# Optimization experiments

Measured on AMD Instinct MI355X. Metric: run time of the kernel, lower is better.

The kernel has to match this reference:

```python
import jax, jax.numpy as jnp
import numpy as np

B, V, D, NH, DH = 1, 6, 256, 8, 32
L, ZP = 4, 4
BEV = 80
Q = BEV * BEV
SHAPES = [(56, 100), (28, 50), (14, 25), (7, 13)]
N = sum(h * w for h, w in SHAPES)
PAD_H, PAD_W = 448, 800
PC = (-48.0, -48.0, -5.0, 48.0, 48.0, 3.0)
EPS = 1e-5


def _ref3d():
    # get_reference_points + pc_range scaling; the original overwrites the z channel
    # with scaled-x (code bug: ref_3d[...,2:3] = ref_3d[...,:1]*zrange+zmin) -> reproduced faithfully,
    # so all ZP pillar points are identical.
    u = jnp.arange(Q)
    xs = ((u % BEV).astype(jnp.float32) + 0.5) / BEV
    ys = ((u // BEV).astype(jnp.float32) + 0.5) / BEV
    x = xs * (PC[3] - PC[0]) + PC[0]
    y = ys * (PC[4] - PC[1]) + PC[1]
    z = x * (PC[5] - PC[2]) + PC[2]
    p = jnp.stack([x, y, z], -1)  # [Q,3]
    return jnp.broadcast_to(p[None], (ZP, Q, 3))


def _project(l2i):
    # l2i: [B,V,4,4] -> normalized coords [B,V,Q,ZP,2], validity mask [B,V,Q,ZP]
    pts = _ref3d().reshape(-1, 3)
    pts_h = jnp.concatenate([pts, jnp.ones_like(pts[:, :1])], -1)  # [ZP*Q,4]
    ip = jnp.einsum('bvij,nj->bvni', l2i, pts_h)                   # [B,V,ZP*Q,4]
    zc = ip[..., 2]
    xy = ip[..., :2] / jnp.clip(zc, EPS, None)[..., None]
    xn = xy[..., 0] / PAD_W
    yn = xy[..., 1] / PAD_H
    m = (zc > EPS) & (xn > 0) & (xn < 1) & (yn > 0) & (yn < 1)
    coords = jnp.stack([xn, yn], -1).reshape(B, V, ZP, Q, 2).transpose(0, 1, 3, 2, 4)
    mask = m.reshape(B, V, ZP, Q).transpose(0, 1, 3, 2)
    return coords, mask


def _forward(feat0, feat1, feat2, feat3, lidar2img_mat, bev_emb, level_embeds,
             view_embeds, value_W, value_b, off_W, off_b, aw_W, aw_b, out_W, out_b):
    feats = [feat0, feat1, feat2, feat3]
    parts = []
    for l, f in enumerate(feats):
        h, w = SHAPES[l]
        x = f.reshape(B, V, D, h * w).transpose(0, 1, 3, 2)  # [B,V,hw,D]
        x = x + view_embeds[None, :, None, :] + level_embeds[l]
        parts.append(x)
    feat_flat = jnp.concatenate(parts, axis=2)  # [B,V,N,D]

    coords, mask = _project(lidar2img_mat)
    mask_any = mask.any(-1)                                            # [B,V,Q]
    count = jnp.clip(mask_any.sum(1).astype(jnp.float32), 1.0, None)   # [B,Q]

    value = (feat_flat.reshape(B * V, N, D) @ value_W + value_b).reshape(B * V, N, NH, DH)
    off = (bev_emb @ off_W + off_b).reshape(Q, NH, L, ZP, 2)
    aw = jax.nn.softmax((bev_emb @ aw_W + aw_b).reshape(Q, NH, L * ZP), -1).reshape(Q, NH, L, ZP)
    ref = coords.reshape(B * V, Q, ZP, 2)

    out = jnp.zeros((B * V, Q, NH, DH), feat_flat.dtype)
    start = 0
    for l, (h, w) in enumerate(SHAPES):
        v_l = value[:, start:start + h * w].transpose(0, 2, 1, 3).reshape(B * V * NH, h * w, DH)
        start += h * w
        loc = ref[:, :, None, :, :] + off[None, :, :, l] / jnp.array([w, h], feat_flat.dtype)
        loc = loc.transpose(0, 2, 1, 3, 4).reshape(B * V * NH, Q * ZP, 2)
        # grid_sample(align_corners=False, padding='zeros') with grid 2*loc-1
        gx = loc[..., 0] * w - 0.5
        gy = loc[..., 1] * h - 0.5
        x0 = jnp.floor(gx).astype(jnp.int32)
        y0 = jnp.floor(gy).astype(jnp.int32)
        wx1 = gx - x0
        wy1 = gy - y0

        def corner(xi, yi, wt):
            valid = (xi >= 0) & (xi < w) & (yi >= 0) & (yi < h)
            lin = jnp.clip(yi, 0, h - 1) * w + jnp.clip(xi, 0, w - 1)
            g = jnp.take_along_axis(v_l, lin[..., None], axis=1)
            return g * (wt * valid)[..., None]

        s = (corner(x0, y0, (1 - wx1) * (1 - wy1)) + corner(x0 + 1, y0, wx1 * (1 - wy1))
             + corner(x0, y0 + 1, (1 - wx1) * wy1) + corner(x0 + 1, y0 + 1, wx1 * wy1))
        s = s.reshape(B * V, NH, Q, ZP, DH)
        out = out + jnp.einsum('vhqzd,qhz->vqhd', s, aw[:, :, l])

    attn = out.reshape(B, V, Q, D)
    slots = (attn * mask_any[..., None]).sum(1) / count[..., None]
    slots = slots @ out_W + out_b
    return bev_emb[None] + slots  # dropout is identity at inference


def setup_inputs() -> dict:
    key = jax.random.key(0)
    ks = jax.random.split(key, 16)
    s = 0.02
    return {
        'feat0': jax.random.normal(ks[0], (B, V, D) + SHAPES[0], jnp.float32),
        'feat1': jax.random.normal(ks[1], (B, V, D) + SHAPES[1], jnp.float32),
        'feat2': jax.random.normal(ks[2], (B, V, D) + SHAPES[2], jnp.float32),
        'feat3': jax.random.normal(ks[3], (B, V, D) + SHAPES[3], jnp.float32),
        'lidar2img_mat': jax.random.normal(ks[4], (B, V, 4, 4), jnp.float32) * 50.0,
        'bev_emb': jax.random.normal(ks[5], (Q, D), jnp.float32) * s,
        'level_embeds': jax.random.normal(ks[6], (L, D), jnp.float32) * s,
        'view_embeds': jax.random.normal(ks[7], (V, D), jnp.float32) * s,
        'value_W': jax.random.normal(ks[8], (D, D), jnp.float32) * s,
        'value_b': jnp.zeros((D,), jnp.float32),
        'off_W': jax.random.normal(ks[9], (D, NH * L * ZP * 2), jnp.float32) * s,
        'off_b': jnp.zeros((NH * L * ZP * 2,), jnp.float32),
        'aw_W': jax.random.normal(ks[10], (D, NH * L * ZP), jnp.float32) * s,
        'aw_b': jnp.zeros((NH * L * ZP,), jnp.float32),
        'out_W': jax.random.normal(ks[11], (D, D), jnp.float32) * s,
        'out_b': jnp.zeros((D,), jnp.float32),
    }


def reference(feat0, feat1, feat2, feat3, lidar2img_mat, bev_emb, level_embeds,
              view_embeds, value_W, value_b, off_W, off_b, aw_W, aw_b, out_W, out_b):
    return _forward(feat0, feat1, feat2, feat3, lidar2img_mat, bev_emb, level_embeds,
                    view_embeds, value_W, value_b, off_W, off_b, aw_W, aw_b, out_W, out_b)
```

## Files before the change

### kernel.cpp

```cpp
#include <hip/hip_runtime.h>
#include <cstdint>
#include <cstddef>

#define NV 6
#define ND 256
#define NHEAD 8
#define NBEV 80
#define NQ 6400
#define NTOK 7441
#define MROWS (NV * NTOK)
#define FEPS 1e-5f

typedef __attribute__((ext_vector_type(8))) short bfx8;
typedef __attribute__((ext_vector_type(4))) float fx4;

__device__ __forceinline__ unsigned short f2bf(float x) {
    uint32_t u = __builtin_bit_cast(uint32_t, x);
    u += 0x7FFFu + ((u >> 16) & 1u);
    return (unsigned short)(u >> 16);
}
__device__ __forceinline__ float lof(uint32_t u) {
    return __builtin_bit_cast(float, u << 16);
}
__device__ __forceinline__ float hif(uint32_t u) {
    return __builtin_bit_cast(float, u & 0xFFFF0000u);
}

__global__ __launch_bounds__(256) void k_prep(
        const float* __restrict__ l2i, const float* __restrict__ ve,
        const float* __restrict__ le, const float* __restrict__ vW,
        const float* __restrict__ vB, const float* __restrict__ oW,
        const float* __restrict__ aW, const float* __restrict__ outW,
        float2* __restrict__ coords, int* __restrict__ mask,
        unsigned short* __restrict__ vWt, unsigned short* __restrict__ oaWt,
        unsigned short* __restrict__ outWt, float* __restrict__ emb_proj) {
    int bid = blockIdx.x;
    int t = threadIdx.x;
    if (bid < 150) {
        int idx = bid * 256 + t;
        int v = idx / NQ, q = idx - v * NQ;
        float xs = ((float)(q % NBEV) + 0.5f) / (float)NBEV;
        float ys = ((float)(q / NBEV) + 0.5f) / (float)NBEV;
        float x = xs * 96.0f - 48.0f;
        float y = ys * 96.0f - 48.0f;
        float z = x * 8.0f - 5.0f;
        const float* M = l2i + v * 16;
        float ip0 = M[0] * x + M[1] * y + M[2] * z + M[3];
        float ip1 = M[4] * x + M[5] * y + M[6] * z + M[7];
        float ip2 = M[8] * x + M[9] * y + M[10] * z + M[11];
        float dz = fmaxf(ip2, FEPS);
        float xn = ip0 / dz / 800.0f;
        float yn = ip1 / dz / 448.0f;
        bool m = (ip2 > FEPS) && (xn > 0.0f) && (xn < 1.0f) && (yn > 0.0f) && (yn < 1.0f);
        coords[idx] = make_float2(xn, yn);
        mask[idx] = m ? 1 : 0;
    } else if (bid < 406) {
        int e = (bid - 150) * 256 + t;
        int n = e >> 8, k = e & 255;
        vWt[(size_t)n * 256 + k] = f2bf(vW[(size_t)k * 256 + n]);
    } else if (bid < 662) {
        int e = (bid - 406) * 256 + t;
        int n = e >> 8, k = e & 255;
        oaWt[(size_t)n * 256 + k] = f2bf(oW[(size_t)k * 256 + n]);
    } else if (bid < 790) {
        int e = (bid - 662) * 256 + t;
        int n = e >> 8, k = e & 255;
        oaWt[(size_t)(256 + n) * 256 + k] = f2bf(aW[(size_t)k * 128 + n]);
    } else if (bid < 1046) {
        int e = (bid - 790) * 256 + t;
        int n = e >> 8, k = e & 255;
        outWt[(size_t)n * 256 + k] = f2bf(outW[(size_t)k * 256 + n]);
    } else {
        int blk = bid - 1046;
        int v = blk >> 2, l = blk & 3;
        float acc = vB[t];
        for (int d = 0; d < ND; ++d)
            acc += (ve[v * ND + d] + le[l * ND + d]) * vW[d * ND + t];
        emb_proj[blk * ND + t] = acc;
    }
}

__global__ __launch_bounds__(256) void k_gemms(
        const float* __restrict__ f0, const float* __restrict__ f1,
        const float* __restrict__ f2, const float* __restrict__ f3,
        const unsigned short* __restrict__ vWt, const float* __restrict__ emb_proj,
        unsigned short* __restrict__ value,
        const float* __restrict__ bev, const unsigned short* __restrict__ oaWt,
        const float* __restrict__ oB, const float* __restrict__ aB,
        float* __restrict__ off, float* __restrict__ aw_pre) {
    __shared__ unsigned short As[128][40];
    __shared__ unsigned short Bs[128][40];
    __shared__ const float* rowptr[128];
    __shared__ int rowstride[128];
    __shared__ int rowemb[128];
    int bid = blockIdx.x;
    int t = threadIdx.x;
    int lane = t & 63, w = t >> 6;
    int wm = w >> 1, wn = w & 1;
    int lr = lane & 15, lk = lane >> 4;

    fx4 acc[4][4];
#pragma unroll
    for (int i = 0; i < 4; ++i)
#pragma unroll
        for (int j = 0; j < 4; ++j) acc[i][j] = (fx4)0.0f;

    if (bid < 698) {
        int m0 = (bid >> 1) * 128, c0 = (bid & 1) * 128;
        if (t < 128) {
            int m = m0 + t;
            if (m >= MROWS) m = MROWS - 1;
            int v = m / NTOK, n = m - v * NTOK;
            int l, p, hw;
            const float* base;
            if (n < 5600)      { l = 0; p = n;        hw = 5600; base = f0; }
            else if (n < 7000) { l = 1; p = n - 5600; hw = 1400; base = f1; }
            else if (n < 7350) { l = 2; p = n - 7000; hw = 350;  base = f2; }
            else               { l = 3; p = n - 7350; hw = 91;   base = f3; }
            rowptr[t] = base + (size_t)v * ND * hw + p;
            rowstride[t] = hw;
            rowemb[t] = v * 4 + l;
        }
        __syncthreads();
        int mA = t & 127, kg = t >> 7;
        const unsigned short* bp = vWt + (size_t)(c0 + (t >> 1)) * 256 + (t & 1) * 16;
        int br = t >> 1, bc = (t & 1) * 16;
        const float* rp = rowptr[mA];
        int rs = rowstride[mA];
        for (int k0 = 0; k0 < 256; k0 += 32) {
            float va[16];
#pragma unroll
            for (int i = 0; i < 16; ++i)
                va[i] = rp[(size_t)(k0 + kg * 16 + i) * rs];
            bfx8 lo8, hi8;
#pragma unroll
            for (int i = 0; i < 8; ++i) {
                lo8[i] = (short)f2bf(va[i]);
                hi8[i] = (short)f2bf(va[i + 8]);
            }
            *(bfx8*)&As[mA][kg * 16] = lo8;
            *(bfx8*)&As[mA][kg * 16 + 8] = hi8;
            *(bfx8*)&Bs[br][bc] = *(const bfx8*)(bp + k0);
            *(bfx8*)&Bs[br][bc + 8] = *(const bfx8*)(bp + k0 + 8);
            __syncthreads();
            bfx8 af[4], bf[4];
#pragma unroll
            for (int f = 0; f < 4; ++f) {
                af[f] = *(bfx8*)&As[wm * 64 + f * 16 + lr][lk * 8];
                bf[f] = *(bfx8*)&Bs[wn * 64 + f * 16 + lr][lk * 8];
            }
#pragma unroll
            for (int fm = 0; fm < 4; ++fm)
#pragma unroll
                for (int fn = 0; fn < 4; ++fn)
                    acc[fm][fn] = __builtin_amdgcn_mfma_f32_16x16x32_bf16(
                        af[fm], bf[fn], acc[fm][fn], 0, 0, 0);
            __syncthreads();
        }
#pragma unroll
        for (int fm = 0; fm < 4; ++fm) {
#pragma unroll
            for (int fn = 0; fn < 4; ++fn) {
                int col = c0 + wn * 64 + fn * 16 + lr;
#pragma unroll
                for (int r = 0; r < 4; ++r) {
                    int rl = wm * 64 + fm * 16 + lk * 4 + r;
                    int m = m0 + rl;
                    if (m < MROWS) {
                        float e = emb_proj[(size_t)rowemb[rl] * ND + col];
                        value[(size_t)m * ND + col] = f2bf(acc[fm][fn][r] + e);
                    }
                }
            }
        }
    } else {
        int r6 = bid - 698;
        int m0 = (r6 / 3) * 128, c0 = (r6 % 3) * 128;
        const float* ap = bev + (size_t)(m0 + (t >> 1)) * 256 + (t & 1) * 16;
        const unsigned short* bp = oaWt + (size_t)(c0 + (t >> 1)) * 256 + (t & 1) * 16;
        int sr = t >> 1, sc = (t & 1) * 16;
        for (int k0 = 0; k0 < 256; k0 += 32) {
            float va[16];
#pragma unroll
            for (int i = 0; i < 4; ++i)
                *(float4*)&va[i * 4] = *(const float4*)(ap + k0 + i * 4);
            bfx8 lo8, hi8;
#pragma unroll
            for (int i = 0; i < 8; ++i) {
                lo8[i] = (short)f2bf(va[i]);
                hi8[i] = (short)f2bf(va[i + 8]);
            }
            *(bfx8*)&As[sr][sc] = lo8;
            *(bfx8*)&As[sr][sc + 8] = hi8;
            *(bfx8*)&Bs[sr][sc] = *(const bfx8*)(bp + k0);
            *(bfx8*)&Bs[sr][sc + 8] = *(const bfx8*)(bp + k0 + 8);
            __syncthreads();
            bfx8 af[4], bf[4];
#pragma unroll
            for (int f = 0; f < 4; ++f) {
                af[f] = *(bfx8*)&As[wm * 64 + f * 16 + lr][lk * 8];
                bf[f] = *(bfx8*)&Bs[wn * 64 + f * 16 + lr][lk * 8];
            }
#pragma unroll
            for (int fm = 0; fm < 4; ++fm)
#pragma unroll
                for (int fn = 0; fn < 4; ++fn)
                    acc[fm][fn] = __builtin_amdgcn_mfma_f32_16x16x32_bf16(
                        af[fm], bf[fn], acc[fm][fn], 0, 0, 0);
            __syncthreads();
        }
        if (c0 < 256) {
#pragma unroll
            for (int fm = 0; fm < 4; ++fm) {
#pragma unroll
                for (int fn = 0; fn < 4; ++fn) {
                    int col = c0 + wn * 64 + fn * 16 + lr;
                    float bs = oB[col];
#pragma unroll
                    for (int r = 0; r < 4; ++r) {
                        int m = m0 + wm * 64 + fm * 16 + lk * 4 + r;
                        off[(size_t)m * 256 + col] = acc[fm][fn][r] + bs;
                    }
                }
            }
        } else {
#pragma unroll
            for (int fm = 0; fm < 4; ++fm) {
#pragma unroll
                for (int fn = 0; fn < 4; ++fn) {
                    int col = wn * 64 + fn * 16 + lr;
                    float bs = aB[col];
#pragma unroll
                    for (int r = 0; r < 4; ++r) {
                        int m = m0 + wm * 64 + fm * 16 + lk * 4 + r;
                        aw_pre[(size_t)m * 128 + col] = acc[fm][fn][r] + bs;
                    }
                }
            }
        }
    }
}

#define SQB 2
__global__ __launch_bounds__(256) void k_sample(
        const float2* __restrict__ coords, const int* __restrict__ mask,
        const float* __restrict__ off, const float* __restrict__ awlog,
        const unsigned short* __restrict__ value, float* __restrict__ slots) {
    __shared__ float aw_s[SQB][128];
    __shared__ int  lin_s[SQB][NV][128][4];
    __shared__ float w_s[SQB][NV][128][4];
    __shared__ float2 cxy_s[SQB][NV];
    __shared__ int msk_s[SQB][NV];

    int b = blockIdx.x;
    int lb = (b & 7) * (NQ / SQB / 8) + (b >> 3);
    int q0 = lb * SQB;
    int t = threadIdx.x;
    if (t < SQB * NV) {
        int qq = t / NV, v = t - qq * NV;
        msk_s[qq][v] = mask[v * NQ + q0 + qq];
        cxy_s[qq][v] = coords[v * NQ + q0 + qq];
    }
    {
        int qq = t >> 7, c2 = t & 127;
        aw_s[qq][c2] = awlog[(size_t)(q0 + qq) * 128 + c2];
    }
    __syncthreads();
    if (t < SQB * NHEAD) {
        int qq = t >> 3, h = t & 7;
        float* p = &aw_s[qq][h * 16];
        float mx = p[0];
#pragma unroll
        for (int i = 1; i < 16; ++i) mx = fmaxf(mx, p[i]);
        float e[16];
        float s = 0.0f;
#pragma unroll
        for (int i = 0; i < 16; ++i) { e[i] = __expf(p[i] - mx); s += e[i]; }
        float inv = 1.0f / s;
#pragma unroll
        for (int i = 0; i < 16; ++i) p[i] = e[i] * inv;
    }
    __syncthreads();

    const int LW[4] = {100, 50, 25, 13};
    const int LH[4] = {56, 28, 14, 7};
    const int LST[4] = {0, 5600, 7000, 7350};
    for (int idx = t; idx < SQB * NV * 128; idx += 256) {
        int c2 = idx & 127;
        int rem = idx >> 7;
        int qq = rem / NV, v = rem - qq * NV;
        if (!msk_s[qq][v]) continue;
        int ll = (c2 >> 2) & 3;
        int iwl = LW[ll], ihl = LH[ll], st = LST[ll];
        float wl = (float)iwl, hl = (float)ihl;
        float2 o2 = *(const float2*)&off[(size_t)(q0 + qq) * 256 + 2 * c2];
        float2 cc = cxy_s[qq][v];
        float gx = cc.x * wl + o2.x - 0.5f;
        float gy = cc.y * hl + o2.y - 0.5f;
        float fxf = floorf(gx), fyf = floorf(gy);
        int x0 = (int)fxf, y0 = (int)fyf;
        float wx = gx - fxf, wy = gy - fyf;
        bool bx0 = (unsigned)x0 < (unsigned)iwl;
        bool bx1 = (unsigned)(x0 + 1) < (unsigned)iwl;
        bool by0 = (unsigned)y0 < (unsigned)ihl;
        bool by1 = (unsigned)(y0 + 1) < (unsigned)ihl;
        int cx0 = min(max(x0, 0), iwl - 1);
        int cx1 = min(max(x0 + 1, 0), iwl - 1);
        int cy0 = min(max(y0, 0), ihl - 1);
        int cy1 = min(max(y0 + 1, 0), ihl - 1);
        float wa = aw_s[qq][c2];
        int r0 = st + cy0 * iwl, r1 = st + cy1 * iwl;
        lin_s[qq][v][c2][0] = r0 + cx0;
        lin_s[qq][v][c2][1] = r0 + cx1;
        lin_s[qq][v][c2][2] = r1 + cx0;
        lin_s[qq][v][c2][3] = r1 + cx1;
        w_s[qq][v][c2][0] = (bx0 && by0) ? (1.0f - wx) * (1.0f - wy) * wa : 0.0f;
        w_s[qq][v][c2][1] = (bx1 && by0) ? wx * (1.0f - wy) * wa : 0.0f;
        w_s[qq][v][c2][2] = (bx0 && by1) ? (1.0f - wx) * wy * wa : 0.0f;
        w_s[qq][v][c2][3] = (bx1 && by1) ? wx * wy * wa : 0.0f;
    }
    __syncthreads();

    int qq = t >> 7, cp = t & 127;
    int hb = (cp >> 4) * 16;
    float acc0 = 0.0f, acc1 = 0.0f;
    int cnt = 0;
#pragma unroll
    for (int v = 0; v < NV; ++v) cnt += msk_s[qq][v];
    for (int v = 0; v < NV; ++v) {
        if (!msk_s[qq][v]) continue;
        const uint32_t* vb = (const uint32_t*)(value + (size_t)v * NTOK * 256) + cp;
#pragma unroll
        for (int ci = 0; ci < 16; ++ci) {
            int c2 = hb + ci;
            int4 lin = *(const int4*)lin_s[qq][v][c2];
            float4 ww = *(const float4*)w_s[qq][v][c2];
            uint32_t u0 = vb[(size_t)lin.x * 128];
            uint32_t u1 = vb[(size_t)lin.y * 128];
            uint32_t u2 = vb[(size_t)lin.z * 128];
            uint32_t u3 = vb[(size_t)lin.w * 128];
            acc0 += ww.x * lof(u0) + ww.y * lof(u1) + ww.z * lof(u2) + ww.w * lof(u3);
            acc1 += ww.x * hif(u0) + ww.y * hif(u1) + ww.z * hif(u2) + ww.w * hif(u3);
        }
    }
    float invc = 1.0f / fmaxf((float)cnt, 1.0f);
    *(float2*)&slots[(size_t)(q0 + qq) * 256 + 2 * cp] = make_float2(acc0 * invc, acc1 * invc);
}

__global__ __launch_bounds__(256) void k_out(
        const float* __restrict__ A, const unsigned short* __restrict__ Bt,
        const float* __restrict__ bias, const float* __restrict__ addsrc,
        float* __restrict__ out) {
    __shared__ unsigned short As[128][40];
    __shared__ unsigned short Bs[128][40];
    int t = threadIdx.x;
    int m0 = blockIdx.x * 128, c0 = blockIdx.y * 128;
    int lane = t & 63, w = t >> 6;
    int wm = w >> 1, wn = w & 1;
    int lr = lane & 15, lk = lane >> 4;
    const float* ap = A + (size_t)(m0 + (t >> 1)) * 256 + (t & 1) * 16;
    const unsigned short* bp = Bt + (size_t)(c0 + (t >> 1)) * 256 + (t & 1) * 16;
    int sr = t >> 1, sc = (t & 1) * 16;
    fx4 acc[4][4];
#pragma unroll
    for (int i = 0; i < 4; ++i)
#pragma unroll
        for (int j = 0; j < 4; ++j) acc[i][j] = (fx4)0.0f;
    for (int k0 = 0; k0 < 256; k0 += 32) {
        float va[16];
#pragma unroll
        for (int i = 0; i < 4; ++i)
            *(float4*)&va[i * 4] = *(const float4*)(ap + k0 + i * 4);
        bfx8 lo8, hi8;
#pragma unroll
        for (int i = 0; i < 8; ++i) {
            lo8[i] = (short)f2bf(va[i]);
            hi8[i] = (short)f2bf(va[i + 8]);
        }
        *(bfx8*)&As[sr][sc] = lo8;
        *(bfx8*)&As[sr][sc + 8] = hi8;
        *(bfx8*)&Bs[sr][sc] = *(const bfx8*)(bp + k0);
        *(bfx8*)&Bs[sr][sc + 8] = *(const bfx8*)(bp + k0 + 8);
        __syncthreads();
        bfx8 af[4], bf[4];
#pragma unroll
        for (int f = 0; f < 4; ++f) {
            af[f] = *(bfx8*)&As[wm * 64 + f * 16 + lr][lk * 8];
            bf[f] = *(bfx8*)&Bs[wn * 64 + f * 16 + lr][lk * 8];
        }
#pragma unroll
        for (int fm = 0; fm < 4; ++fm)
#pragma unroll
            for (int fn = 0; fn < 4; ++fn)
                acc[fm][fn] = __builtin_amdgcn_mfma_f32_16x16x32_bf16(
                    af[fm], bf[fn], acc[fm][fn], 0, 0, 0);
        __syncthreads();
    }
#pragma unroll
    for (int fm = 0; fm < 4; ++fm) {
#pragma unroll
        for (int fn = 0; fn < 4; ++fn) {
            int col = c0 + wn * 64 + fn * 16 + lr;
            float bs = bias[col];
#pragma unroll
            for (int r = 0; r < 4; ++r) {
                int m = m0 + wm * 64 + fm * 16 + lk * 4 + r;
                out[(size_t)m * 256 + col] =
                    acc[fm][fn][r] + bs + addsrc[(size_t)m * 256 + col];
            }
        }
    }
}

extern "C" void kernel_launch(void* const* d_in, const int* in_sizes, int n_in,
                              void* d_out, int out_size, void* d_ws, size_t ws_size,
                              hipStream_t stream) {
    const float* f0   = (const float*)d_in[0];
    const float* f1   = (const float*)d_in[1];
    const float* f2   = (const float*)d_in[2];
    const float* f3   = (const float*)d_in[3];
    const float* l2i  = (const float*)d_in[4];
    const float* bev  = (const float*)d_in[5];
    const float* le   = (const float*)d_in[6];
    const float* ve   = (const float*)d_in[7];
    const float* vW   = (const float*)d_in[8];
    const float* vB   = (const float*)d_in[9];
    const float* oW   = (const float*)d_in[10];
    const float* oB   = (const float*)d_in[11];
    const float* aW   = (const float*)d_in[12];
    const float* aB   = (const float*)d_in[13];
    const float* outW = (const float*)d_in[14];
    const float* outB = (const float*)d_in[15];
    float* out = (float*)d_out;

    char* ws = (char*)d_ws;
    size_t o = 0;
    auto alloc = [&](size_t bytes) {
        void* p = ws + o;
        o += (bytes + 255) & ~(size_t)255;
        return p;
    };
    float2* coords   = (float2*)alloc((size_t)NV * NQ * sizeof(float2));
    int*    mask     = (int*)alloc((size_t)NV * NQ * sizeof(int));
    float*  emb_proj = (float*)alloc((size_t)24 * ND * sizeof(float));
    float*  off      = (float*)alloc((size_t)NQ * 256 * sizeof(float));
    float*  aw_pre   = (float*)alloc((size_t)NQ * 128 * sizeof(float));
    float*  slots    = (float*)alloc((size_t)NQ * 256 * sizeof(float));
    unsigned short* value = (unsigned short*)alloc((size_t)MROWS * ND * sizeof(short));
    unsigned short* vWt   = (unsigned short*)alloc((size_t)256 * 256 * sizeof(short));
    unsigned short* oaWt  = (unsigned short*)alloc((size_t)384 * 256 * sizeof(short));
    unsigned short* outWt = (unsigned short*)alloc((size_t)256 * 256 * sizeof(short));

    k_prep<<<1070, 256, 0, stream>>>(l2i, ve, le, vW, vB, oW, aW, outW,
                                     coords, mask, vWt, oaWt, outWt, emb_proj);
    k_gemms<<<848, 256, 0, stream>>>(f0, f1, f2, f3, vWt, emb_proj, value,
                                     bev, oaWt, oB, aB, off, aw_pre);
    k_sample<<<NQ / SQB, 256, 0, stream>>>(coords, mask, off, aw_pre, value, slots);
    dim3 gout(NQ / 128, 2);
    k_out<<<gout, 256, 0, stream>>>(slots, outWt, outB, bev, out);
}
```

Before: 199.6 us.

## Halve GEMM M-tiles, swizzle block order, coalesce weight transpose, pack sampler LDS to fp16/u16

All three GEMM paths now use 64-row M tiles instead of 128, which doubles the block count and halves the per-thread accumulators. k_gemms also gets an XCD-aware block index remap (b&7 chunking). The weight-transpose loops in k_prep swap index roles so the fp32 source reads are coalesced. The sampler stores its corner indices as 16-bit and its bilinear weights as fp16 in LDS, cutting shared memory to raise occupancy at some cost in weight precision and a risk of index overflow.

```diff
diff --git a/kernel.cpp b/kernel.cpp
--- a/kernel.cpp
+++ b/kernel.cpp
@@ -11,8 +11,16 @@
 #define MROWS (NV * NTOK)
 #define FEPS 1e-5f
 
+#define VROWT 698
+#define VBLKS (VROWT * 2)
+#define OABLKS 300
+#define GBLKS (VBLKS + OABLKS)
+#define GCHUNK (GBLKS / 8)
+
 typedef __attribute__((ext_vector_type(8))) short bfx8;
 typedef __attribute__((ext_vector_type(4))) float fx4;
+typedef __attribute__((ext_vector_type(4))) _Float16 hx4;
+typedef __attribute__((ext_vector_type(4))) unsigned short usx4;
 
 __device__ __forceinline__ unsigned short f2bf(float x) {
     uint32_t u = __builtin_bit_cast(uint32_t, x);
@@ -56,19 +64,19 @@
         mask[idx] = m ? 1 : 0;
     } else if (bid < 406) {
         int e = (bid - 150) * 256 + t;
-        int n = e >> 8, k = e & 255;
+        int k = e >> 8, n = e & 255;
         vWt[(size_t)n * 256 + k] = f2bf(vW[(size_t)k * 256 + n]);
     } else if (bid < 662) {
         int e = (bid - 406) * 256 + t;
-        int n = e >> 8, k = e & 255;
+        int k = e >> 8, n = e & 255;
         oaWt[(size_t)n * 256 + k] = f2bf(oW[(size_t)k * 256 + n]);
     } else if (bid < 790) {
         int e = (bid - 662) * 256 + t;
-        int n = e >> 8, k = e & 255;
+        int k = e >> 7, n = e & 127;
         oaWt[(size_t)(256 + n) * 256 + k] = f2bf(aW[(size_t)k * 128 + n]);
     } else if (bid < 1046) {
         int e = (bid - 790) * 256 + t;
-        int n = e >> 8, k = e & 255;
+        int k = e >> 8, n = e & 255;
         outWt[(size_t)n * 256 + k] = f2bf(outW[(size_t)k * 256 + n]);
     } else {
         int blk = bid - 1046;
@@ -88,26 +96,28 @@
         const float* __restrict__ bev, const unsigned short* __restrict__ oaWt,
         const float* __restrict__ oB, const float* __restrict__ aB,
         float* __restrict__ off, float* __restrict__ aw_pre) {
-    __shared__ unsigned short As[128][40];
+    __shared__ unsigned short As[64][40];
     __shared__ unsigned short Bs[128][40];
-    __shared__ const float* rowptr[128];
-    __shared__ int rowstride[128];
-    __shared__ int rowemb[128];
-    int bid = blockIdx.x;
+    __shared__ const float* rowptr[64];
+    __shared__ int rowstride[64];
+    __shared__ int rowemb[64];
+    int b = blockIdx.x;
+    int lb = (b & 7) * GCHUNK + (b >> 3);
     int t = threadIdx.x;
     int lane = t & 63, w = t >> 6;
     int wm = w >> 1, wn = w & 1;
     int lr = lane & 15, lk = lane >> 4;
-
-    fx4 acc[4][4];
-#pragma unroll
-    for (int i = 0; i < 4; ++i)
+    int mA = t & 63, kg = t >> 6;
+
+    fx4 acc[2][4];
+#pragma unroll
+    for (int i = 0; i < 2; ++i)
 #pragma unroll
         for (int j = 0; j < 4; ++j) acc[i][j] = (fx4)0.0f;
 
-    if (bid < 698) {
-        int m0 = (bid >> 1) * 128, c0 = (bid & 1) * 128;
-        if (t < 128) {
+    if (lb < VBLKS) {
+        int m0 = (lb >> 1) * 64, c0 = (lb & 1) * 128;
+        if (t < 64) {
             int m = m0 + t;
             if (m >= MROWS) m = MROWS - 1;
             int v = m / NTOK, n = m - v * NTOK;
@@ -122,35 +132,30 @@
             rowemb[t] = v * 4 + l;
         }
         __syncthreads();
-        int mA = t & 127, kg = t >> 7;
         const unsigned short* bp = vWt + (size_t)(c0 + (t >> 1)) * 256 + (t & 1) * 16;
-        int br = t >> 1, bc = (t & 1) * 16;
         const float* rp = rowptr[mA];
         int rs = rowstride[mA];
         for (int k0 = 0; k0 < 256; k0 += 32) {
-            float va[16];
-#pragma unroll
-            for (int i = 0; i < 16; ++i)
-                va[i] = rp[(size_t)(k0 + kg * 16 + i) * rs];
-            bfx8 lo8, hi8;
-#pragma unroll
-            for (int i = 0; i < 8; ++i) {
-                lo8[i] = (short)f2bf(va[i]);
-                hi8[i] = (short)f2bf(va[i + 8]);
-            }
-            *(bfx8*)&As[mA][kg * 16] = lo8;
-            *(bfx8*)&As[mA][kg * 16 + 8] = hi8;
-            *(bfx8*)&Bs[br][bc] = *(const bfx8*)(bp + k0);
-            *(bfx8*)&Bs[br][bc + 8] = *(const bfx8*)(bp + k0 + 8);
+            float va[8];
+#pragma unroll
+            for (int i = 0; i < 8; ++i)
+                va[i] = rp[(size_t)(k0 + kg * 8 + i) * rs];
+            bfx8 a8;
+#pragma unroll
+            for (int i = 0; i < 8; ++i) a8[i] = (short)f2bf(va[i]);
+            *(bfx8*)&As[mA][kg * 8] = a8;
+            *(bfx8*)&Bs[t >> 1][(t & 1) * 16] = *(const bfx8*)(bp + k0);
+            *(bfx8*)&Bs[t >> 1][(t & 1) * 16 + 8] = *(const bfx8*)(bp + k0 + 8);
             __syncthreads();
-            bfx8 af[4], bf[4];
-#pragma unroll
-            for (int f = 0; f < 4; ++f) {
-                af[f] = *(bfx8*)&As[wm * 64 + f * 16 + lr][lk * 8];
+            bfx8 af[2], bf[4];
+#pragma unroll
+            for (int f = 0; f < 2; ++f)
+                af[f] = *(bfx8*)&As[wm * 32 + f * 16 + lr][lk * 8];
+#pragma unroll
+            for (int f = 0; f < 4; ++f)
                 bf[f] = *(bfx8*)&Bs[wn * 64 + f * 16 + lr][lk * 8];
-            }
-#pragma unroll
-            for (int fm = 0; fm < 4; ++fm)
+#pragma unroll
+            for (int fm = 0; fm < 2; ++fm)
 #pragma unroll
                 for (int fn = 0; fn < 4; ++fn)
                     acc[fm][fn] = __builtin_amdgcn_mfma_f32_16x16x32_bf16(
@@ -158,13 +163,13 @@
             __syncthreads();
         }
 #pragma unroll
-        for (int fm = 0; fm < 4; ++fm) {
+        for (int fm = 0; fm < 2; ++fm) {
 #pragma unroll
             for (int fn = 0; fn < 4; ++fn) {
                 int col = c0 + wn * 64 + fn * 16 + lr;
 #pragma unroll
                 for (int r = 0; r < 4; ++r) {
-                    int rl = wm * 64 + fm * 16 + lk * 4 + r;
+                    int rl = wm * 32 + fm * 16 + lk * 4 + r;
                     int m = m0 + rl;
                     if (m < MROWS) {
                         float e = emb_proj[(size_t)rowemb[rl] * ND + col];
@@ -174,35 +179,30 @@
             }
         }
     } else {
-        int r6 = bid - 698;
-        int m0 = (r6 / 3) * 128, c0 = (r6 % 3) * 128;
-        const float* ap = bev + (size_t)(m0 + (t >> 1)) * 256 + (t & 1) * 16;
+        int r6 = lb - VBLKS;
+        int m0 = (r6 / 3) * 64, c0 = (r6 % 3) * 128;
+        const float* ap = bev + (size_t)(m0 + mA) * 256 + kg * 8;
         const unsigned short* bp = oaWt + (size_t)(c0 + (t >> 1)) * 256 + (t & 1) * 16;
-        int sr = t >> 1, sc = (t & 1) * 16;
         for (int k0 = 0; k0 < 256; k0 += 32) {
-            float va[16];
-#pragma unroll
-            for (int i = 0; i < 4; ++i)
-                *(float4*)&va[i * 4] = *(const float4*)(ap + k0 + i * 4);
-            bfx8 lo8, hi8;
-#pragma unroll
-            for (int i = 0; i < 8; ++i) {
-                lo8[i] = (short)f2bf(va[i]);
-                hi8[i] = (short)f2bf(va[i + 8]);
-            }
-            *(bfx8*)&As[sr][sc] = lo8;
-            *(bfx8*)&As[sr][sc + 8] = hi8;
-            *(bfx8*)&Bs[sr][sc] = *(const bfx8*)(bp + k0);
-            *(bfx8*)&Bs[sr][sc + 8] = *(const bfx8*)(bp + k0 + 8);
+            float va[8];
+            *(float4*)&va[0] = *(const float4*)(ap + k0);
+            *(float4*)&va[4] = *(const float4*)(ap + k0 + 4);
+            bfx8 a8;
+#pragma unroll
+            for (int i = 0; i < 8; ++i) a8[i] = (short)f2bf(va[i]);
+            *(bfx8*)&As[mA][kg * 8] = a8;
+            *(bfx8*)&Bs[t >> 1][(t & 1) * 16] = *(const bfx8*)(bp + k0);
+            *(bfx8*)&Bs[t >> 1][(t & 1) * 16 + 8] = *(const bfx8*)(bp + k0 + 8);
             __syncthreads();
-            bfx8 af[4], bf[4];
-#pragma unroll
-            for (int f = 0; f < 4; ++f) {
-                af[f] = *(bfx8*)&As[wm * 64 + f * 16 + lr][lk * 8];
+            bfx8 af[2], bf[4];
+#pragma unroll
+            for (int f = 0; f < 2; ++f)
+                af[f] = *(bfx8*)&As[wm * 32 + f * 16 + lr][lk * 8];
+#pragma unroll
+            for (int f = 0; f < 4; ++f)
                 bf[f] = *(bfx8*)&Bs[wn * 64 + f * 16 + lr][lk * 8];
-            }
-#pragma unroll
-            for (int fm = 0; fm < 4; ++fm)
+#pragma unroll
+            for (int fm = 0; fm < 2; ++fm)
 #pragma unroll
                 for (int fn = 0; fn < 4; ++fn)
                     acc[fm][fn] = __builtin_amdgcn_mfma_f32_16x16x32_bf16(
@@ -211,28 +211,28 @@
         }
         if (c0 < 256) {
 #pragma unroll
-            for (int fm = 0; fm < 4; ++fm) {
+            for (int fm = 0; fm < 2; ++fm) {
 #pragma unroll
                 for (int fn = 0; fn < 4; ++fn) {
                     int col = c0 + wn * 64 + fn * 16 + lr;
                     float bs = oB[col];
 #pragma unroll
                     for (int r = 0; r < 4; ++r) {
-                        int m = m0 + wm * 64 + fm * 16 + lk * 4 + r;
+                        int m = m0 + wm * 32 + fm * 16 + lk * 4 + r;
                         off[(size_t)m * 256 + col] = acc[fm][fn][r] + bs;
                     }
                 }
             }
         } else {
 #pragma unroll
-            for (int fm = 0; fm < 4; ++fm) {
+            for (int fm = 0; fm < 2; ++fm) {
 #pragma unroll
                 for (int fn = 0; fn < 4; ++fn) {
                     int col = wn * 64 + fn * 16 + lr;
                     float bs = aB[col];
 #pragma unroll
                     for (int r = 0; r < 4; ++r) {
-                        int m = m0 + wm * 64 + fm * 16 + lk * 4 + r;
+                        int m = m0 + wm * 32 + fm * 16 + lk * 4 + r;
                         aw_pre[(size_t)m * 128 + col] = acc[fm][fn][r] + bs;
                     }
                 }
@@ -247,8 +247,8 @@
         const float* __restrict__ off, const float* __restrict__ awlog,
         const unsigned short* __restrict__ value, float* __restrict__ slots) {
     __shared__ float aw_s[SQB][128];
-    __shared__ int  lin_s[SQB][NV][128][4];
-    __shared__ float w_s[SQB][NV][128][4];
+    __shared__ unsigned short lin_s[SQB][NV][128][4];
+    __shared__ _Float16 w_s[SQB][NV][128][4];
     __shared__ float2 cxy_s[SQB][NV];
     __shared__ int msk_s[SQB][NV];
 
@@ -310,14 +310,18 @@
         int cy1 = min(max(y0 + 1, 0), ihl - 1);
         float wa = aw_s[qq][c2];
         int r0 = st + cy0 * iwl, r1 = st + cy1 * iwl;
-        lin_s[qq][v][c2][0] = r0 + cx0;
-        lin_s[qq][v][c2][1] = r0 + cx1;
-        lin_s[qq][v][c2][2] = r1 + cx0;
-        lin_s[qq][v][c2][3] = r1 + cx1;
-        w_s[qq][v][c2][0] = (bx0 && by0) ? (1.0f - wx) * (1.0f - wy) * wa : 0.0f;
-        w_s[qq][v][c2][1] = (bx1 && by0) ? wx * (1.0f - wy) * wa : 0.0f;
-        w_s[qq][v][c2][2] = (bx0 && by1) ? (1.0f - wx) * wy * wa : 0.0f;
-        w_s[qq][v][c2][3] = (bx1 && by1) ? wx * wy * wa : 0.0f;
+        usx4 lin;
+        lin.x = (unsigned short)(r0 + cx0);
+        lin.y = (unsigned short)(r0 + cx1);
+        lin.z = (unsigned short)(r1 + cx0);
+        lin.w = (unsigned short)(r1 + cx1);
+        hx4 ww;
+        ww.x = (_Float16)((bx0 && by0) ? (1.0f - wx) * (1.0f - wy) * wa : 0.0f);
+        ww.y = (_Float16)((bx1 && by0) ? wx * (1.0f - wy) * wa : 0.0f);
+        ww.z = (_Float16)((bx0 && by1) ? (1.0f - wx) * wy * wa : 0.0f);
+        ww.w = (_Float16)((bx1 && by1) ? wx * wy * wa : 0.0f);
+        *(usx4*)lin_s[qq][v][c2] = lin;
+        *(hx4*)w_s[qq][v][c2] = ww;
     }
     __syncthreads();
 
@@ -333,14 +337,16 @@
 #pragma unroll
         for (int ci = 0; ci < 16; ++ci) {
             int c2 = hb + ci;
-            int4 lin = *(const int4*)lin_s[qq][v][c2];
-            float4 ww = *(const float4*)w_s[qq][v][c2];
+            usx4 lin = *(const usx4*)lin_s[qq][v][c2];
+            hx4 wh = *(const hx4*)w_s[qq][v][c2];
             uint32_t u0 = vb[(size_t)lin.x * 128];
             uint32_t u1 = vb[(size_t)lin.y * 128];
             uint32_t u2 = vb[(size_t)lin.z * 128];
             uint32_t u3 = vb[(size_t)lin.w * 128];
-            acc0 += ww.x * lof(u0) + ww.y * lof(u1) + ww.z * lof(u2) + ww.w * lof(u3);
-            acc1 += ww.x * hif(u0) + ww.y * hif(u1) + ww.z * hif(u2) + ww.w * hif(u3);
+            float w0 = (float)wh.x, w1 = (float)wh.y;
+            float w2 = (float)wh.z, w3 = (float)wh.w;
+            acc0 += w0 * lof(u0) + w1 * lof(u1) + w2 * lof(u2) + w3 * lof(u3);
+            acc1 += w0 * hif(u0) + w1 * hif(u1) + w2 * hif(u2) + w3 * hif(u3);
         }
     }
     float invc = 1.0f / fmaxf((float)cnt, 1.0f);
@@ -351,45 +357,41 @@
         const float* __restrict__ A, const unsigned short* __restrict__ Bt,
         const float* __restrict__ bias, const float* __restrict__ addsrc,
         float* __restrict__ out) {
-    __shared__ unsigned short As[128][40];
+    __shared__ unsigned short As[64][40];
     __shared__ unsigned short Bs[128][40];
     int t = threadIdx.x;
-    int m0 = blockIdx.x * 128, c0 = blockIdx.y * 128;
+    int m0 = blockIdx.x * 64, c0 = blockIdx.y * 128;
     int lane = t & 63, w = t >> 6;
     int wm = w >> 1, wn = w & 1;
     int lr = lane & 15, lk = lane >> 4;
-    const float* ap = A + (size_t)(m0 + (t >> 1)) * 256 + (t & 1) * 16;
+    int mA = t & 63, kg = t >> 6;
+    const float* ap = A + (size_t)(m0 + mA) * 256 + kg * 8;
     const unsigned short* bp = Bt + (size_t)(c0 + (t >> 1)) * 256 + (t & 1) * 16;
-    int sr = t >> 1, sc = (t & 1) * 16;
-    fx4 acc[4][4];
-#pragma unroll
-    for (int i = 0; i < 4; ++i)
+    fx4 acc[2][4];
+#pragma unroll
+    for (int i = 0; i < 2; ++i)
 #pragma unroll
         for (int j = 0; j < 4; ++j) acc[i][j] = (fx4)0.0f;
     for (int k0 = 0; k0 < 256; k0 += 32) {
-        float va[16];
-#pragma unroll
-        for (int i = 0; i < 4; ++i)
-            *(float4*)&va[i * 4] = *(const float4*)(ap + k0 + i * 4);
-        bfx8 lo8, hi8;
-#pragma unroll
-        for (int i = 0; i < 8; ++i) {
-            lo8[i] = (short)f2bf(va[i]);
-            hi8[i] = (short)f2bf(va[i + 8]);
-        }
-        *(bfx8*)&As[sr][sc] = lo8;
-        *(bfx8*)&As[sr][sc + 8] = hi8;
-        *(bfx8*)&Bs[sr][sc] = *(const bfx8*)(bp + k0);
-        *(bfx8*)&Bs[sr][sc + 8] = *(const bfx8*)(bp + k0 + 8);
+        float va[8];
+        *(float4*)&va[0] = *(const float4*)(ap + k0);
+        *(float4*)&va[4] = *(const float4*)(ap + k0 + 4);
+        bfx8 a8;
+#pragma unroll
+        for (int i = 0; i < 8; ++i) a8[i] = (short)f2bf(va[i]);
+        *(bfx8*)&As[mA][kg * 8] = a8;
+        *(bfx8*)&Bs[t >> 1][(t & 1) * 16] = *(const bfx8*)(bp + k0);
+        *(bfx8*)&Bs[t >> 1][(t & 1) * 16 + 8] = *(const bfx8*)(bp + k0 + 8);
         __syncthreads();
-        bfx8 af[4], bf[4];
-#pragma unroll
-        for (int f = 0; f < 4; ++f) {
-            af[f] = *(bfx8*)&As[wm * 64 + f * 16 + lr][lk * 8];
+        bfx8 af[2], bf[4];
+#pragma unroll
+        for (int f = 0; f < 2; ++f)
+            af[f] = *(bfx8*)&As[wm * 32 + f * 16 + lr][lk * 8];
+#pragma unroll
+        for (int f = 0; f < 4; ++f)
             bf[f] = *(bfx8*)&Bs[wn * 64 + f * 16 + lr][lk * 8];
-        }
-#pragma unroll
-        for (int fm = 0; fm < 4; ++fm)
+#pragma unroll
+        for (int fm = 0; fm < 2; ++fm)
 #pragma unroll
             for (int fn = 0; fn < 4; ++fn)
                 acc[fm][fn] = __builtin_amdgcn_mfma_f32_16x16x32_bf16(
@@ -397,14 +399,14 @@
         __syncthreads();
     }
 #pragma unroll
-    for (int fm = 0; fm < 4; ++fm) {
+    for (int fm = 0; fm < 2; ++fm) {
 #pragma unroll
         for (int fn = 0; fn < 4; ++fn) {
             int col = c0 + wn * 64 + fn * 16 + lr;
             float bs = bias[col];
 #pragma unroll
             for (int r = 0; r < 4; ++r) {
-                int m = m0 + wm * 64 + fm * 16 + lk * 4 + r;
+                int m = m0 + wm * 32 + fm * 16 + lk * 4 + r;
                 out[(size_t)m * 256 + col] =
                     acc[fm][fn][r] + bs + addsrc[(size_t)m * 256 + col];
             }
@@ -453,9 +455,9 @@
 
     k_prep<<<1070, 256, 0, stream>>>(l2i, ve, le, vW, vB, oW, aW, outW,
                                      coords, mask, vWt, oaWt, outWt, emb_proj);
-    k_gemms<<<848, 256, 0, stream>>>(f0, f1, f2, f3, vWt, emb_proj, value,
-                                     bev, oaWt, oB, aB, off, aw_pre);
+    k_gemms<<<GBLKS, 256, 0, stream>>>(f0, f1, f2, f3, vWt, emb_proj, value,
+                                       bev, oaWt, oB, aB, off, aw_pre);
     k_sample<<<NQ / SQB, 256, 0, stream>>>(coords, mask, off, aw_pre, value, slots);
-    dim3 gout(NQ / 128, 2);
+    dim3 gout(NQ / 64, 2);
     k_out<<<gout, 256, 0, stream>>>(slots, outWt, outB, bev, out);
 }
```

Result: slower. 204.6 us (+2.5%).
